# Performance work log

Hardware: AMD Instinct MI355X
Metric: run time of the kernel (lower is better)

The kernel has to match this reference:

```python
import jax, jax.numpy as jnp
import numpy as np

HEADS = 8
DIM_HEAD = 64
SCALE = DIM_HEAD ** -0.5

def layernorm_ch(x, g, eps=1e-5):
    # channel-wise LayerNorm over dim=1 (NCHW), biased variance
    mean = jnp.mean(x, axis=1, keepdims=True)
    var = jnp.var(x, axis=1, keepdims=True)
    return (x - mean) * jax.lax.rsqrt(var + eps) * g[None, :, None, None]

def setup_inputs() -> dict:
    key = jax.random.key(0)
    ks = jax.random.split(key, 4)
    B, C, H, W = 16, 512, 64, 64
    hidden = HEADS * DIM_HEAD
    x = jax.random.normal(ks[0], (B, C, H, W), dtype=jnp.float32)
    w_qkv = jax.random.normal(ks[1], (3 * hidden, C), dtype=jnp.float32) * (C ** -0.5)
    w_out = jax.random.normal(ks[2], (C, hidden), dtype=jnp.float32) * (hidden ** -0.5)
    b_out = jnp.zeros((C,), dtype=jnp.float32)
    g_out = jnp.ones((C,), dtype=jnp.float32)
    g_ln = jnp.ones((C,), dtype=jnp.float32)
    return {"x": x, "w_qkv": w_qkv, "w_out": w_out, "b_out": b_out, "g_out": g_out, "g_ln": g_ln}

def reference(x, w_qkv, w_out, b_out, g_out, g_ln):
    B, C, H, W = x.shape
    n = H * W
    x_norm = layernorm_ch(x, g_ln)
    # 1x1 conv == channel GEMM: [B,3*hidden,H,W]
    qkv = jnp.einsum('oc,bchw->bohw', w_qkv, x_norm)
    q, k, v = jnp.split(qkv, 3, axis=1)
    # b (h d) x y -> b h d n
    def to_heads(t):
        return t.reshape(B, HEADS, DIM_HEAD, n)
    q, k, v = to_heads(q), to_heads(k), to_heads(v)
    q = jax.nn.softmax(q, axis=-2) * SCALE   # softmax over d
    k = jax.nn.softmax(k, axis=-1)           # softmax over n
    v = v / n
    context = jnp.einsum('bhdn,bhen->bhde', k, v)
    out = jnp.einsum('bhde,bhdn->bhen', context, q)
    out = out.reshape(B, HEADS * DIM_HEAD, H, W)
    out = jnp.einsum('oc,bchw->bohw', w_out, out) + b_out[None, :, None, None]
    out = layernorm_ch(out, g_out)
    return out + x
```

## Files before the change

### kernel.cpp

```cpp
#include <hip/hip_runtime.h>
#include <math.h>

#define CCH    512
#define HWN    4096
#define NPIX   65536
#define OC3    1536
#define QSCALE 0.125f
#define LN_EPS 1e-5f

typedef _Float16 h16;
typedef h16  f16x8 __attribute__((ext_vector_type(8)));
typedef float f32x4 __attribute__((ext_vector_type(4)));

__device__ __forceinline__ float waveReduceSum(float v) {
#pragma unroll
    for (int off = 32; off; off >>= 1) v += __shfl_xor(v, off);
    return v;
}

__device__ __forceinline__ void gl_lds16(const void* g, void* l) {
    __builtin_amdgcn_global_load_lds((const __attribute__((address_space(1))) void*)g,
                                     (__attribute__((address_space(3))) void*)l, 16, 0, 0);
}

__global__ __launch_bounds__(64) void prep_w(const float* __restrict__ w_qkv,
                                             const float* __restrict__ g_ln,
                                             const float* __restrict__ w_out,
                                             h16* __restrict__ wg_h,
                                             float* __restrict__ s,
                                             h16* __restrict__ wo_h) {
    const int o = blockIdx.x, lane = threadIdx.x;
    if (o < OC3) {
        float sum = 0.f;
#pragma unroll
        for (int j = 0; j < 8; ++j) {
            const int c = lane + j * 64;
            const float w = w_qkv[(size_t)o * CCH + c] * g_ln[c];
            wg_h[(size_t)o * CCH + c] = (h16)(w * 64.f);
            sum += w;
        }
        sum = waveReduceSum(sum);
        if (lane == 0) s[o] = sum;
    } else {
        const int r = o - OC3;
#pragma unroll
        for (int j = 0; j < 8; ++j) {
            const int c = lane + j * 64;
            wo_h[(size_t)r * CCH + c] = (h16)(w_out[(size_t)r * CCH + c] * 64.f);
        }
    }
}

__global__ __launch_bounds__(256) void transpose_cvt(const float* __restrict__ src,
                                                     h16* __restrict__ dhi,
                                                     float* __restrict__ psum,
                                                     float* __restrict__ psq) {
    __shared__ float tile[64][65];
    __shared__ float ps1[4][64], ps2[4][64];
    const int b = blockIdx.z, c0 = blockIdx.y * 64, p0 = blockIdx.x * 64;
    const int t = threadIdx.x;
    const float* sb = src + ((size_t)b * CCH + c0) * HWN + p0;
    const int rc = t >> 4, cc4 = (t & 15) * 4;
#pragma unroll
    for (int ps = 0; ps < 4; ++ps) {
        const float4 v = *(const float4*)(sb + (size_t)(rc + ps * 16) * HWN + cc4);
        tile[rc + ps * 16][cc4 + 0] = v.x;
        tile[rc + ps * 16][cc4 + 1] = v.y;
        tile[rc + ps * 16][cc4 + 2] = v.z;
        tile[rc + ps * 16][cc4 + 3] = v.w;
    }
    __syncthreads();
    {
        const int q = t >> 6, px = t & 63;
        float s1 = 0.f, s2 = 0.f;
#pragma unroll
        for (int c = q * 16; c < q * 16 + 16; ++c) {
            const float v = tile[c][px];
            s1 += v; s2 += v * v;
        }
        ps1[q][px] = s1; ps2[q][px] = s2;
    }
    const int pr0 = t >> 3, cs = (t & 7) * 8;
#pragma unroll
    for (int ps = 0; ps < 2; ++ps) {
        const int pr = pr0 + ps * 32;
        f16x8 vh;
#pragma unroll
        for (int q = 0; q < 8; ++q) vh[q] = (h16)tile[cs + q][pr];
        const size_t o = ((size_t)b * HWN + p0 + pr) * CCH + c0 + cs;
        *(f16x8*)(dhi + o) = vh;
    }
    __syncthreads();
    if (t < 64) {
        const float s1 = ps1[0][t] + ps1[1][t] + ps1[2][t] + ps1[3][t];
        const float s2 = ps2[0][t] + ps2[1][t] + ps2[2][t] + ps2[3][t];
        const size_t gp = (size_t)b * HWN + p0 + t;
        psum[(size_t)(c0 >> 6) * NPIX + gp] = s1;
        psq [(size_t)(c0 >> 6) * NPIX + gp] = s2;
    }
}

__global__ __launch_bounds__(512) void qkv_gemm(const h16* __restrict__ Ahg,
                                                const h16* __restrict__ Bhg,
                                                const float* __restrict__ sv,
                                                const float* __restrict__ psum,
                                                const float* __restrict__ psq,
                                                h16* __restrict__ qout) {
    __shared__ __align__(16) h16 Ah[8192];
    __shared__ __align__(16) h16 Bh[16384];
    __shared__ float mnS[256], rsS[256];
    const int tid = threadIdx.x;
    const int om = blockIdx.x * 128;
    const int by0 = blockIdx.y;
    const int by  = (by0 & 7) * 32 + (by0 >> 3);
    const int p0  = by * 256;

    const int srow = tid >> 2;
    const int skh  = ((tid & 3) ^ (srow & 3)) * 8;
    const size_t a0 = (size_t)(om + srow) * CCH + skh;
    const size_t b0 = (size_t)(p0 + srow) * CCH + skh;

    const int lane = tid & 63;
    const int wv = tid >> 6;
    const int wm = (wv >> 2) * 64, wn = (wv & 3) * 64;
    const int lr = lane & 15, kg = lane >> 4;
    const int swz = (kg ^ (lr & 3)) * 8;

    f32x4 acc[4][4];
#pragma unroll
    for (int i = 0; i < 4; ++i)
#pragma unroll
        for (int j = 0; j < 4; ++j) acc[i][j] = {0.f, 0.f, 0.f, 0.f};

#define STAGE(KC)                                                          \
    do {                                                                   \
        gl_lds16(Ahg + a0 + (KC),                 Ah + tid * 8);           \
        gl_lds16(Ahg + a0 + (KC) + 32,            Ah + 4096 + tid * 8);    \
        gl_lds16(Bhg + b0 + (KC),                 Bh + tid * 8);           \
        gl_lds16(Bhg + b0 + (KC) + 128 * CCH,     Bh + 4096 + tid * 8);    \
        gl_lds16(Bhg + b0 + (KC) + 32,            Bh + 8192 + tid * 8);    \
        gl_lds16(Bhg + b0 + (KC) + 32 + 128 * CCH, Bh + 12288 + tid * 8);  \
    } while (0)

    STAGE(0);
    if (tid < 256) {
        const int gp = p0 + tid;
        float s1 = 0.f, s2 = 0.f;
#pragma unroll
        for (int cb = 0; cb < 8; ++cb) {
            s1 += psum[(size_t)cb * NPIX + gp];
            s2 += psq [(size_t)cb * NPIX + gp];
        }
        const float m = s1 * (1.f / 512.f);
        float var = s2 * (1.f / 512.f) - m * m;
        var = fmaxf(var, 0.f);
        mnS[tid] = m;
        rsS[tid] = rsqrtf(var + LN_EPS);
    }

#pragma unroll 1
    for (int kc = 0; kc < 512; kc += 64) {
        __syncthreads();
        f16x8 a0f[4], b0f[4], a1f[4], b1f[4];
#pragma unroll
        for (int i = 0; i < 4; ++i) {
            a0f[i] = *(const f16x8*)(Ah + (wm + i * 16 + lr) * 32 + swz);
            b0f[i] = *(const f16x8*)(Bh + (wn + i * 16 + lr) * 32 + swz);
        }
#pragma unroll
        for (int i = 0; i < 4; ++i)
#pragma unroll
            for (int j = 0; j < 4; ++j)
                acc[i][j] = __builtin_amdgcn_mfma_f32_16x16x32_f16(a0f[i], b0f[j], acc[i][j], 0, 0, 0);
#pragma unroll
        for (int i = 0; i < 4; ++i) {
            a1f[i] = *(const f16x8*)(Ah + 4096 + (wm + i * 16 + lr) * 32 + swz);
            b1f[i] = *(const f16x8*)(Bh + 8192 + (wn + i * 16 + lr) * 32 + swz);
        }
        __syncthreads();
        if (kc + 64 < 512) STAGE(kc + 64);
#pragma unroll
        for (int i = 0; i < 4; ++i)
#pragma unroll
            for (int j = 0; j < 4; ++j)
                acc[i][j] = __builtin_amdgcn_mfma_f32_16x16x32_f16(a1f[i], b1f[j], acc[i][j], 0, 0, 0);
    }
#undef STAGE

    const int b = p0 >> 12, hw0 = p0 & 4095;
    float mn[4], rs[4];
#pragma unroll
    for (int j = 0; j < 4; ++j) {
        const int px = wn + j * 16 + lr;
        mn[j] = mnS[px]; rs[j] = rsS[px];
    }
#pragma unroll
    for (int i = 0; i < 4; ++i)
#pragma unroll
        for (int r = 0; r < 4; ++r) {
            const int o = om + wm + i * 16 + kg * 4 + r;
            const float so = sv[o];
            h16* dst = qout + ((size_t)b * OC3 + o) * HWN;
#pragma unroll
            for (int j = 0; j < 4; ++j) {
                const int hw = hw0 + wn + j * 16 + lr;
                dst[hw] = (h16)(rs[j] * (acc[i][j][r] * (1.f / 64.f) - mn[j] * so));
            }
        }
}

__global__ __launch_bounds__(64) void ctx_partial(const h16* __restrict__ qkv16,
                                                  float* __restrict__ ctp) {
    const int bh = blockIdx.y, ci = blockIdx.x;
    const int b = bh >> 3, h = bh & 7;
    const h16* kb = qkv16 + ((size_t)b * OC3 + CCH  + h * 64) * HWN;
    const h16* vb = qkv16 + ((size_t)b * OC3 + 1024 + h * 64) * HWN;
    const int lane = threadIdx.x;
    const int lr = lane & 15, kg = lane >> 4;
    const int nbase = ci * 256 + kg * 8;

    float m[4] = {-1e30f, -1e30f, -1e30f, -1e30f};
#pragma unroll 1
    for (int c = 0; c < 8; ++c) {
        const int n0 = nbase + c * 32;
#pragma unroll
        for (int i = 0; i < 4; ++i) {
            const f16x8 kv = *(const f16x8*)(kb + (size_t)(i * 16 + lr) * HWN + n0);
#pragma unroll
            for (int u = 0; u < 8; ++u) m[i] = fmaxf(m[i], (float)kv[u]);
        }
    }
#pragma unroll
    for (int i = 0; i < 4; ++i) {
        m[i] = fmaxf(m[i], __shfl_xor(m[i], 16));
        m[i] = fmaxf(m[i], __shfl_xor(m[i], 32));
    }

    float z[4] = {0.f, 0.f, 0.f, 0.f};
    f32x4 acc[4][4];
#pragma unroll
    for (int i = 0; i < 4; ++i)
#pragma unroll
        for (int j = 0; j < 4; ++j) acc[i][j] = {0.f, 0.f, 0.f, 0.f};

#pragma unroll 1
    for (int c = 0; c < 8; ++c) {
        const int n0 = nbase + c * 32;
        f16x8 ke[4], vf[4];
#pragma unroll
        for (int j = 0; j < 4; ++j)
            vf[j] = *(const f16x8*)(vb + (size_t)(j * 16 + lr) * HWN + n0);
#pragma unroll
        for (int i = 0; i < 4; ++i) {
            const f16x8 kv = *(const f16x8*)(kb + (size_t)(i * 16 + lr) * HWN + n0);
            f16x8 t;
#pragma unroll
            for (int u = 0; u < 8; ++u) {
                const float e = __expf((float)kv[u] - m[i]);
                z[i] += e;
                t[u] = (h16)e;
            }
            ke[i] = t;
        }
#pragma unroll
        for (int i = 0; i < 4; ++i)
#pragma unroll
            for (int j = 0; j < 4; ++j)
                acc[i][j] = __builtin_amdgcn_mfma_f32_16x16x32_f16(ke[i], vf[j], acc[i][j], 0, 0, 0);
    }
#pragma unroll
    for (int i = 0; i < 4; ++i) {
        z[i] += __shfl_xor(z[i], 16);
        z[i] += __shfl_xor(z[i], 32);
    }
    float* dst = ctp + ((size_t)bh * 16 + ci) * 4224;
#pragma unroll
    for (int i = 0; i < 4; ++i)
#pragma unroll
        for (int j = 0; j < 4; ++j)
#pragma unroll
            for (int r = 0; r < 4; ++r)
                dst[(i * 16 + kg * 4 + r) * 64 + j * 16 + lr] = acc[i][j][r];
    if (kg == 0)
#pragma unroll
        for (int i = 0; i < 4; ++i) {
            dst[4096 + i * 16 + lr] = z[i];
            dst[4160 + i * 16 + lr] = m[i];
        }
}

__global__ __launch_bounds__(256) void ctx_reduce(const float* __restrict__ ctp,
                                                  float* __restrict__ ct) {
    __shared__ float w[16][64];
    __shared__ float rz[64];
    const int bh = blockIdx.x;
    const int tid = threadIdx.x;
    const float* src = ctp + (size_t)bh * 16 * 4224;
    if (tid < 64) {
        float M = -1e30f;
#pragma unroll
        for (int ci = 0; ci < 16; ++ci)
            M = fmaxf(M, src[(size_t)ci * 4224 + 4160 + tid]);
        float Z = 0.f;
#pragma unroll
        for (int ci = 0; ci < 16; ++ci) {
            const float ww = __expf(src[(size_t)ci * 4224 + 4160 + tid] - M);
            w[ci][tid] = ww;
            Z += ww * src[(size_t)ci * 4224 + 4096 + tid];
        }
        rz[tid] = 1.f / Z;
    }
    __syncthreads();
    float* dst = ct + (size_t)bh * 4096;
    for (int e4 = tid * 4; e4 < 4096; e4 += 1024) {
        const int d = e4 >> 6;
        float4 sum = make_float4(0.f, 0.f, 0.f, 0.f);
#pragma unroll
        for (int ci = 0; ci < 16; ++ci) {
            const float4 v = *(const float4*)(src + (size_t)ci * 4224 + e4);
            const float ww = w[ci][d];
            sum.x += ww * v.x; sum.y += ww * v.y;
            sum.z += ww * v.z; sum.w += ww * v.w;
        }
        const float r = rz[d];
        sum.x *= r; sum.y *= r; sum.z *= r; sum.w *= r;
        *(float4*)(dst + e4) = sum;
    }
}

__global__ __launch_bounds__(256) void attn_out(const h16* __restrict__ qkv16,
                                                const float* __restrict__ ct,
                                                h16* __restrict__ at) {
    __shared__ float cts[64][68];
    __shared__ float qt[64][68];

    const int bh = blockIdx.y, ci = blockIdx.x;
    const int b = bh >> 3, h = bh & 7;
    const h16* qb = qkv16 + ((size_t)b * OC3 + h * 64) * HWN;
    const int tid = threadIdx.x;

    for (int i4 = tid * 4; i4 < 4096; i4 += 1024) {
        const float4 v = *(const float4*)(ct + (size_t)bh * 4096 + i4);
        *(float4*)&cts[i4 >> 6][i4 & 63] = v;
    }

    const int d  = tid >> 2;
    const int te = tid & 15, tn = tid >> 4;
    const int rn = tid >> 2, d0q = (tid & 3) * 16;

    for (int t = 0; t < 8; ++t) {
        const int n0 = ci * 512 + t * 64;
        __syncthreads();
#pragma unroll
        for (int jj = 0; jj < 2; ++jj) {
            const int nn = (tid & 3) * 8 + jj * 32;
            const f16x8 qv = *(const f16x8*)(qb + (size_t)d * HWN + n0 + nn);
#pragma unroll
            for (int u = 0; u < 8; ++u) qt[nn + u][d] = (float)qv[u];
        }
        __syncthreads();
        {
            float mx = -1e30f;
#pragma unroll
            for (int dd = 0; dd < 16; ++dd) mx = fmaxf(mx, qt[rn][d0q + dd]);
            mx = fmaxf(mx, __shfl_xor(mx, 1));
            mx = fmaxf(mx, __shfl_xor(mx, 2));
            float sm = 0.f;
#pragma unroll
            for (int dd = 0; dd < 16; ++dd) sm += __expf(qt[rn][d0q + dd] - mx);
            sm += __shfl_xor(sm, 1);
            sm += __shfl_xor(sm, 2);
            const float sc = 512.f * QSCALE / sm;
#pragma unroll
            for (int dd = 0; dd < 16; ++dd)
                qt[rn][d0q + dd] = __expf(qt[rn][d0q + dd] - mx) * sc;
        }
        __syncthreads();
        float acc[4][4];
#pragma unroll
        for (int i = 0; i < 4; ++i)
#pragma unroll
            for (int j = 0; j < 4; ++j) acc[i][j] = 0.f;
#pragma unroll
        for (int dd = 0; dd < 64; ++dd) {
            float cv[4];
            *(float4*)cv = *(const float4*)&cts[dd][te * 4];
            const float q0 = qt[tn * 4 + 0][dd];
            const float q1 = qt[tn * 4 + 1][dd];
            const float q2 = qt[tn * 4 + 2][dd];
            const float q3 = qt[tn * 4 + 3][dd];
#pragma unroll
            for (int i = 0; i < 4; ++i) {
                acc[i][0] = fmaf(cv[i], q0, acc[i][0]);
                acc[i][1] = fmaf(cv[i], q1, acc[i][1]);
                acc[i][2] = fmaf(cv[i], q2, acc[i][2]);
                acc[i][3] = fmaf(cv[i], q3, acc[i][3]);
            }
        }
        __syncthreads();
#pragma unroll
        for (int i = 0; i < 4; ++i)
#pragma unroll
            for (int j = 0; j < 4; ++j)
                qt[tn * 4 + j][te * 4 + i] = acc[i][j];
        __syncthreads();
        {
            const int px = tid >> 2, e0 = (tid & 3) * 16;
            f16x8 vh0, vh1;
#pragma unroll
            for (int u = 0; u < 8; ++u) {
                vh0[u] = (h16)qt[px][e0 + u];
                vh1[u] = (h16)qt[px][e0 + 8 + u];
            }
            const size_t o = ((size_t)b * HWN + n0 + px) * CCH + h * 64 + e0;
            *(f16x8*)(at + o)     = vh0;
            *(f16x8*)(at + o + 8) = vh1;
        }
    }
}

__global__ __launch_bounds__(512) void out_fused(const h16* __restrict__ wo_hi,
                                                 const h16* __restrict__ at,
                                                 const float* __restrict__ b_out,
                                                 const float* __restrict__ g_out,
                                                 const float* __restrict__ x,
                                                 float* __restrict__ out) {
    __shared__ __align__(16) h16 Alds[512 * 32];
    __shared__ __align__(16) h16 Blds[128 * 32];
    __shared__ float red1[4][128], red2[4][128];
    __shared__ float mnS[128], rsS[128];

    const int tid = threadIdx.x;
    const int p0 = blockIdx.x * 128;
    const int b = p0 >> 12, hw0 = p0 & 4095;

    const int trow = tid >> 2;
    const int skh  = ((tid & 3) ^ (trow & 3)) * 8;
    const size_t aoff = (size_t)trow * CCH + skh;
    const size_t boff = (size_t)p0 * CCH + aoff;
    const int wofs = (tid >> 6) * 512;

    const int wv = tid >> 6;
    const int wm = (wv >> 1) * 128, wn = (wv & 1) * 64;
    const int lane = tid & 63;
    const int lr = lane & 15, kg = lane >> 4;
    const int swz = (kg ^ (lr & 3)) * 8;

    f32x4 acc[8][4];
#pragma unroll
    for (int i = 0; i < 8; ++i)
#pragma unroll
        for (int j = 0; j < 4; ++j) acc[i][j] = {0.f, 0.f, 0.f, 0.f};

#define STAGEF(S)                                                           \
    do {                                                                    \
        const int kc_ = (S) * 32;                                           \
        gl_lds16(wo_hi + aoff + kc_,               Alds + wofs);            \
        gl_lds16(wo_hi + aoff + kc_ + 128 * CCH,   Alds + 4096 + wofs);     \
        gl_lds16(wo_hi + aoff + kc_ + 256 * CCH,   Alds + 8192 + wofs);     \
        gl_lds16(wo_hi + aoff + kc_ + 384 * CCH,   Alds + 12288 + wofs);    \
        gl_lds16(at + boff + kc_,                  Blds + wofs);            \
    } while (0)

    STAGEF(0);
#pragma unroll 1
    for (int s = 0; s < 16; ++s) {
        __syncthreads();
        f16x8 af[8], bf[4];
#pragma unroll
        for (int i = 0; i < 8; ++i)
            af[i] = *(const f16x8*)(Alds + (wm + i * 16 + lr) * 32 + swz);
#pragma unroll
        for (int j = 0; j < 4; ++j)
            bf[j] = *(const f16x8*)(Blds + (wn + j * 16 + lr) * 32 + swz);
        __syncthreads();
        if (s < 15) STAGEF(s + 1);
#pragma unroll
        for (int i = 0; i < 8; ++i)
#pragma unroll
            for (int j = 0; j < 4; ++j)
                acc[i][j] = __builtin_amdgcn_mfma_f32_16x16x32_f16(af[i], bf[j], acc[i][j], 0, 0, 0);
    }
#undef STAGEF

#pragma unroll
    for (int i = 0; i < 8; ++i) {
        const int o = wm + i * 16 + kg * 4;
        const float4 bb = *(const float4*)(b_out + o);
#pragma unroll
        for (int j = 0; j < 4; ++j) {
            acc[i][j][0] = acc[i][j][0] * (1.f / 134217728.f) + bb.x;
            acc[i][j][1] = acc[i][j][1] * (1.f / 134217728.f) + bb.y;
            acc[i][j][2] = acc[i][j][2] * (1.f / 134217728.f) + bb.z;
            acc[i][j][3] = acc[i][j][3] * (1.f / 134217728.f) + bb.w;
        }
    }
    float s1[4], s2[4];
#pragma unroll
    for (int j = 0; j < 4; ++j) {
        s1[j] = 0.f; s2[j] = 0.f;
#pragma unroll
        for (int i = 0; i < 8; ++i)
#pragma unroll
            for (int r = 0; r < 4; ++r) {
                const float v = acc[i][j][r];
                s1[j] += v; s2[j] += v * v;
            }
        s1[j] += __shfl_xor(s1[j], 16); s1[j] += __shfl_xor(s1[j], 32);
        s2[j] += __shfl_xor(s2[j], 16); s2[j] += __shfl_xor(s2[j], 32);
    }
    if (kg == 0) {
#pragma unroll
        for (int j = 0; j < 4; ++j) {
            red1[wv >> 1][wn + j * 16 + lr] = s1[j];
            red2[wv >> 1][wn + j * 16 + lr] = s2[j];
        }
    }
    __syncthreads();
    if (tid < 128) {
        const float S1 = red1[0][tid] + red1[1][tid] + red1[2][tid] + red1[3][tid];
        const float S2 = red2[0][tid] + red2[1][tid] + red2[2][tid] + red2[3][tid];
        const float m = S1 * (1.f / 512.f);
        float var = S2 * (1.f / 512.f) - m * m;
        var = fmaxf(var, 0.f);
        mnS[tid] = m;
        rsS[tid] = rsqrtf(var + LN_EPS);
    }
    __syncthreads();
    float mj[4], rj[4];
#pragma unroll
    for (int j = 0; j < 4; ++j) {
        const int px = wn + j * 16 + lr;
        mj[j] = mnS[px]; rj[j] = rsS[px];
    }
#pragma unroll
    for (int i = 0; i < 8; ++i) {
        const int o = wm + i * 16 + kg * 4;
        const float4 gg = *(const float4*)(g_out + o);
#pragma unroll
        for (int r = 0; r < 4; ++r) {
            const float g = (r == 0) ? gg.x : (r == 1) ? gg.y : (r == 2) ? gg.z : gg.w;
            const float* xr = x + ((size_t)b * CCH + o + r) * HWN + hw0 + wn;
            float* dr = out + ((size_t)b * CCH + o + r) * HWN + hw0 + wn;
#pragma unroll
            for (int j = 0; j < 4; ++j) {
                const int c = j * 16 + lr;
                dr[c] = (acc[i][j][r] - mj[j]) * rj[j] * g + xr[c];
            }
        }
    }
}

extern "C" void kernel_launch(void* const* d_in, const int* in_sizes, int n_in,
                              void* d_out, int out_size, void* d_ws, size_t ws_size,
                              hipStream_t stream) {
    (void)in_sizes; (void)n_in; (void)out_size;
    const float* x     = (const float*)d_in[0];
    const float* w_qkv = (const float*)d_in[1];
    const float* w_out = (const float*)d_in[2];
    const float* b_out = (const float*)d_in[3];
    const float* g_out = (const float*)d_in[4];
    const float* g_ln  = (const float*)d_in[5];
    float* out = (float*)d_out;
    float* ws  = (float*)d_ws;

    float* s    = ws;
    float* ct   = s + OC3;
    float* ctp  = ct + 524288;
    float* psum = ctp;
    float* psq  = psum + 524288;
    h16*  wg_hi = (h16*)(ctp + 8650752);
    h16*  wo_hi = wg_hi + 786432;
    h16*  qkv16 = wo_hi + 262144;
    h16*  at    = qkv16 + 100663296;
    h16*  xt_hi = (h16*)d_out;

    const size_t need = 76809728ULL * 4ULL;
    if (ws_size < need) return;

    prep_w       <<<2048, 64, 0, stream>>>(w_qkv, g_ln, w_out, wg_hi, s, wo_hi);
    transpose_cvt<<<dim3(64, 8, 16), 256, 0, stream>>>(x, xt_hi, psum, psq);
    qkv_gemm     <<<dim3(12, 256), 512, 0, stream>>>(wg_hi, xt_hi,
                                                     s, psum, psq, qkv16);
    ctx_partial  <<<dim3(16, 128), 64, 0, stream>>>(qkv16, ctp);
    ctx_reduce   <<<128, 256, 0, stream>>>(ctp, ct);
    attn_out     <<<dim3(8, 128), 256, 0, stream>>>(qkv16, ct, at);
    out_fused    <<<512, 512, 0, stream>>>(wo_hi, at,
                                           b_out, g_out, x, out);
}
```

Measured before the change: 433.4 us.

## Use MFMA f16 for context-times-query product in attn_out

```diff
diff --git a/kernel.cpp b/kernel.cpp
--- a/kernel.cpp
+++ b/kernel.cpp
@@ -10,6 +10,7 @@
 
 typedef _Float16 h16;
 typedef h16  f16x8 __attribute__((ext_vector_type(8)));
+typedef h16  f16x4 __attribute__((ext_vector_type(4)));
 typedef float f32x4 __attribute__((ext_vector_type(4)));
 
 __device__ __forceinline__ float waveReduceSum(float v) {
@@ -290,7 +291,7 @@
 }
 
 __global__ __launch_bounds__(256) void ctx_reduce(const float* __restrict__ ctp,
-                                                  float* __restrict__ ct) {
+                                                  h16* __restrict__ ctt) {
     __shared__ float w[16][64];
     __shared__ float rz[64];
     const int bh = blockIdx.x;
@@ -311,9 +312,9 @@
         rz[tid] = 1.f / Z;
     }
     __syncthreads();
-    float* dst = ct + (size_t)bh * 4096;
+    h16* dstt = ctt + (size_t)bh * 4096;
     for (int e4 = tid * 4; e4 < 4096; e4 += 1024) {
-        const int d = e4 >> 6;
+        const int d = e4 >> 6, e0 = e4 & 63;
         float4 sum = make_float4(0.f, 0.f, 0.f, 0.f);
 #pragma unroll
         for (int ci = 0; ci < 16; ++ci) {
@@ -323,29 +324,30 @@
             sum.z += ww * v.z; sum.w += ww * v.w;
         }
         const float r = rz[d];
-        sum.x *= r; sum.y *= r; sum.z *= r; sum.w *= r;
-        *(float4*)(dst + e4) = sum;
+        dstt[(e0 + 0) * 64 + d] = (h16)(sum.x * r);
+        dstt[(e0 + 1) * 64 + d] = (h16)(sum.y * r);
+        dstt[(e0 + 2) * 64 + d] = (h16)(sum.z * r);
+        dstt[(e0 + 3) * 64 + d] = (h16)(sum.w * r);
     }
 }
 
 __global__ __launch_bounds__(256) void attn_out(const h16* __restrict__ qkv16,
-                                                const float* __restrict__ ct,
+                                                const h16* __restrict__ ctt,
                                                 h16* __restrict__ at) {
-    __shared__ float cts[64][68];
-    __shared__ float qt[64][68];
+    __shared__ __align__(16) h16 qt[64][72];
 
     const int bh = blockIdx.y, ci = blockIdx.x;
     const int b = bh >> 3, h = bh & 7;
     const h16* qb = qkv16 + ((size_t)b * OC3 + h * 64) * HWN;
     const int tid = threadIdx.x;
-
-    for (int i4 = tid * 4; i4 < 4096; i4 += 1024) {
-        const float4 v = *(const float4*)(ct + (size_t)bh * 4096 + i4);
-        *(float4*)&cts[i4 >> 6][i4 & 63] = v;
-    }
+    const int lane = tid & 63, wv = tid >> 6;
+    const int lr = lane & 15, kg = lane >> 4;
+
+    const h16* cb = ctt + (size_t)bh * 4096 + (wv * 16 + lr) * 64 + kg * 8;
+    f16x8 af0 = *(const f16x8*)(cb);
+    f16x8 af1 = *(const f16x8*)(cb + 32);
 
     const int d  = tid >> 2;
-    const int te = tid & 15, tn = tid >> 4;
     const int rn = tid >> 2, d0q = (tid & 3) * 16;
 
     for (int t = 0; t < 8; ++t) {
@@ -356,62 +358,56 @@
             const int nn = (tid & 3) * 8 + jj * 32;
             const f16x8 qv = *(const f16x8*)(qb + (size_t)d * HWN + n0 + nn);
 #pragma unroll
-            for (int u = 0; u < 8; ++u) qt[nn + u][d] = (float)qv[u];
+            for (int u = 0; u < 8; ++u) qt[nn + u][d] = qv[u];
         }
         __syncthreads();
         {
+            float qv[16];
             float mx = -1e30f;
 #pragma unroll
-            for (int dd = 0; dd < 16; ++dd) mx = fmaxf(mx, qt[rn][d0q + dd]);
+            for (int dd = 0; dd < 16; ++dd) {
+                qv[dd] = (float)qt[rn][d0q + dd];
+                mx = fmaxf(mx, qv[dd]);
+            }
             mx = fmaxf(mx, __shfl_xor(mx, 1));
             mx = fmaxf(mx, __shfl_xor(mx, 2));
             float sm = 0.f;
 #pragma unroll
-            for (int dd = 0; dd < 16; ++dd) sm += __expf(qt[rn][d0q + dd] - mx);
+            for (int dd = 0; dd < 16; ++dd) {
+                qv[dd] = __expf(qv[dd] - mx);
+                sm += qv[dd];
+            }
             sm += __shfl_xor(sm, 1);
             sm += __shfl_xor(sm, 2);
             const float sc = 512.f * QSCALE / sm;
 #pragma unroll
             for (int dd = 0; dd < 16; ++dd)
-                qt[rn][d0q + dd] = __expf(qt[rn][d0q + dd] - mx) * sc;
-        }
-        __syncthreads();
-        float acc[4][4];
-#pragma unroll
-        for (int i = 0; i < 4; ++i)
-#pragma unroll
-            for (int j = 0; j < 4; ++j) acc[i][j] = 0.f;
-#pragma unroll
-        for (int dd = 0; dd < 64; ++dd) {
-            float cv[4];
-            *(float4*)cv = *(const float4*)&cts[dd][te * 4];
-            const float q0 = qt[tn * 4 + 0][dd];
-            const float q1 = qt[tn * 4 + 1][dd];
-            const float q2 = qt[tn * 4 + 2][dd];
-            const float q3 = qt[tn * 4 + 3][dd];
-#pragma unroll
-            for (int i = 0; i < 4; ++i) {
-                acc[i][0] = fmaf(cv[i], q0, acc[i][0]);
-                acc[i][1] = fmaf(cv[i], q1, acc[i][1]);
-                acc[i][2] = fmaf(cv[i], q2, acc[i][2]);
-                acc[i][3] = fmaf(cv[i], q3, acc[i][3]);
-            }
-        }
-        __syncthreads();
-#pragma unroll
-        for (int i = 0; i < 4; ++i)
-#pragma unroll
-            for (int j = 0; j < 4; ++j)
-                qt[tn * 4 + j][te * 4 + i] = acc[i][j];
+                qt[rn][d0q + dd] = (h16)(qv[dd] * sc);
+        }
+        __syncthreads();
+        f32x4 acc4[4];
+#pragma unroll
+        for (int j = 0; j < 4; ++j) acc4[j] = {0.f, 0.f, 0.f, 0.f};
+#pragma unroll
+        for (int j = 0; j < 4; ++j) {
+            const f16x8 bf0 = *(const f16x8*)(&qt[j * 16 + lr][kg * 8]);
+            const f16x8 bf1 = *(const f16x8*)(&qt[j * 16 + lr][32 + kg * 8]);
+            acc4[j] = __builtin_amdgcn_mfma_f32_16x16x32_f16(af0, bf0, acc4[j], 0, 0, 0);
+            acc4[j] = __builtin_amdgcn_mfma_f32_16x16x32_f16(af1, bf1, acc4[j], 0, 0, 0);
+        }
+        __syncthreads();
+#pragma unroll
+        for (int j = 0; j < 4; ++j) {
+            f16x4 o4;
+            o4[0] = (h16)acc4[j][0]; o4[1] = (h16)acc4[j][1];
+            o4[2] = (h16)acc4[j][2]; o4[3] = (h16)acc4[j][3];
+            *(f16x4*)(&qt[j * 16 + lr][wv * 16 + kg * 4]) = o4;
+        }
         __syncthreads();
         {
             const int px = tid >> 2, e0 = (tid & 3) * 16;
-            f16x8 vh0, vh1;
-#pragma unroll
-            for (int u = 0; u < 8; ++u) {
-                vh0[u] = (h16)qt[px][e0 + u];
-                vh1[u] = (h16)qt[px][e0 + 8 + u];
-            }
+            const f16x8 vh0 = *(const f16x8*)(&qt[px][e0]);
+            const f16x8 vh1 = *(const f16x8*)(&qt[px][e0 + 8]);
             const size_t o = ((size_t)b * HWN + n0 + px) * CCH + h * 64 + e0;
             *(f16x8*)(at + o)     = vh0;
             *(f16x8*)(at + o + 8) = vh1;
@@ -565,8 +561,8 @@
     float* ws  = (float*)d_ws;
 
     float* s    = ws;
-    float* ct   = s + OC3;
-    float* ctp  = ct + 524288;
+    h16*  ctt   = (h16*)(s + OC3);
+    float* ctp  = s + OC3 + 524288;
     float* psum = ctp;
     float* psq  = psum + 524288;
     h16*  wg_hi = (h16*)(ctp + 8650752);
@@ -583,8 +579,8 @@
     qkv_gemm     <<<dim3(12, 256), 512, 0, stream>>>(wg_hi, xt_hi,
                                                      s, psum, psq, qkv16);
     ctx_partial  <<<dim3(16, 128), 64, 0, stream>>>(qkv16, ctp);
-    ctx_reduce   <<<128, 256, 0, stream>>>(ctp, ct);
-    attn_out     <<<dim3(8, 128), 256, 0, stream>>>(qkv16, ct, at);
+    ctx_reduce   <<<128, 256, 0, stream>>>(ctp, ctt);
+    attn_out     <<<dim3(8, 128), 256, 0, stream>>>(qkv16, ctt, at);
     out_fused    <<<512, 512, 0, stream>>>(wo_hi, at,
                                            b_out, g_out, x, out);
 }
```

New measurement: 387.6 us. 10.6% less time.
